# Performance work log

Hardware: AMD Instinct MI355X
Metric: run time of the kernel (lower is better)

## Reference

```python
import jax, jax.numpy as jnp
import numpy as np
from jax import lax
from jax.scipy.special import logsumexp

INSIZE = 256
NBASE = 4
SIZE = 2 * NBASE * (NBASE + 1)  # 40


def setup_inputs() -> dict:
    key = jax.random.key(0)
    kx, kw, kb = jax.random.split(key, 3)
    x = jax.random.normal(kx, (2048, 256, INSIZE), dtype=jnp.float32)
    W = jax.random.normal(kw, (SIZE, INSIZE), dtype=jnp.float32) / np.sqrt(INSIZE)
    b = 0.5 * jax.random.normal(kb, (SIZE,), dtype=jnp.float32)
    return {"x": x, "W": W, "b": b}


def global_norm_flipflop(scores):
    # scores: (T, N, C) with C = 2*nbase*(nbase+1)
    T, N, C = scores.shape
    nbase = int(np.sqrt(C / 2))
    assert 2 * nbase * (nbase + 1) == C

    fwd0 = jnp.zeros((N, 2 * nbase), dtype=scores.dtype)
    logZ0 = logsumexp(fwd0, axis=1, keepdims=True)  # (N, 1) = log(2*nbase)
    fwd0 = fwd0 - logZ0

    def step(carry, sc_t):
        fwd, logZ = carry
        # (N, nbase+1, 2*nbase): transition scores into each destination row
        sc = fwd[:, None, :] + sc_t.reshape(N, nbase + 1, 2 * nbase)
        base1 = logsumexp(sc[:, :nbase], axis=2)  # flip states (N, nbase)
        base2 = jnp.logaddexp(sc[:, nbase, :nbase], sc[:, nbase, nbase:])  # flop (N, nbase)
        new_state = jnp.concatenate([base1, base2], axis=1)  # (N, 2*nbase)
        factors = logsumexp(new_state, axis=1, keepdims=True)
        return (new_state - factors, logZ + factors), None

    (_, logZ), _ = lax.scan(step, (fwd0, logZ0), scores)
    return scores - logZ / T  # broadcast (N,1) over (T,N,C)


def reference(x, W, b):
    y = 5.0 * jnp.tanh(x @ W.T + b)  # (T, N, 40)
    return global_norm_flipflop(y)
```

## Files before the change

kernel.cpp:

```cpp
#include <hip/hip_runtime.h>
#include <hip/hip_bf16.h>

#define T_DIM 2048
#define N_DIM 256
#define K_DIM 256
#define C_DIM 40
#define CHUNK 32
#define NCHUNK 64
#define NSUPER (T_DIM * N_DIM / 64)

#define LOG2E_F 1.44269504088896340736f
#define LN2_F   0.69314718055994530942f
#define NEGBIG  (-1.0e30f)

typedef short bf16x8 __attribute__((ext_vector_type(8)));
typedef float f32x4  __attribute__((ext_vector_type(4)));

__device__ __forceinline__ float fexp2(float x) { return exp2f(x); }
__device__ __forceinline__ float flog2(float x) { return log2f(x); }
__device__ __forceinline__ float frcp(float x) { return __frcp_rn(x); }

__device__ __forceinline__ unsigned int pk2(float a, float b)
{
    __hip_bfloat162 h = __float22bfloat162_rn(make_float2(a, b));
    unsigned int r;
    __builtin_memcpy(&r, &h, sizeof(r));
    return r;
}

__device__ __forceinline__ uint4 pack8u(float4 lo, float4 hi)
{
    uint4 t;
    t.x = pk2(lo.x, lo.y);
    t.y = pk2(lo.z, lo.w);
    t.z = pk2(hi.x, hi.y);
    t.w = pk2(hi.z, hi.w);
    return t;
}

__device__ __forceinline__ bf16x8 as_bf16x8(uint4 u)
{
    bf16x8 r;
    __builtin_memcpy(&r, &u, sizeof(r));
    return r;
}

__device__ __forceinline__ unsigned short bf16r(float v)
{
    return (unsigned short)(pk2(v, 0.0f) & 0xffffu);
}

__device__ __forceinline__ float bl(unsigned int w) { return __uint_as_float(w << 16); }
__device__ __forceinline__ float bh(unsigned int w) { return __uint_as_float(w & 0xffff0000u); }

__device__ __forceinline__ float tanh5(float v)
{
    const float e = fexp2(fabsf(v) * (2.0f * LOG2E_F));
    const float t = 1.0f - 2.0f * frcp(e + 1.0f);
    return 5.0f * copysignf(t, v);
}

__global__ __launch_bounds__(256) void k0_pack(
    const float* __restrict__ W, uint4* __restrict__ wfrag)
{
    const int f    = blockIdx.x * 256 + threadIdx.x;
    const int l    = f & 63;
    const int frag = f >> 6;
    const int nt   = frag % 3;
    const int ks   = frag / 3;
    const int col  = nt * 16 + (l & 15);
    const int kg   = l >> 4;
    float4 lo = make_float4(0, 0, 0, 0), hi = lo;
    if (col < C_DIM) {
        const float* wp = W + (size_t)col * K_DIM + ks * 32 + kg * 8;
        lo = *(const float4*)wp;
        hi = *(const float4*)(wp + 4);
    }
    wfrag[frag * 64 + l] = pack8u(lo, hi);
}

__global__ __launch_bounds__(256, 4) void k1_gemm_tanh(
    const float* __restrict__ x, const uint4* __restrict__ wfrag,
    const float* __restrict__ b, unsigned short* __restrict__ yb)
{
    __shared__ __align__(16) unsigned char xl[64 * 512];

    const int tid  = threadIdx.x;
    const int wave = tid >> 6;
    const int lane = tid & 63;
    const int lr   = lane & 15;
    const int kg   = lane >> 4;
    const int mt   = wave;

    const float bc0 = b[lr];
    const float bc1 = b[16 + lr];
    const float bc2 = (lr < 8) ? b[32 + lr] : 0.0f;

    const int rbase = (mt * 16 + lr) * 512;
    const int swz   = (lr & 7) << 4;

#pragma unroll 1
    for (int st = blockIdx.x; st < NSUPER; st += 1024) {
        const float4* __restrict__ xg4 =
            (const float4*)(x + (size_t)st * 64 * K_DIM);
#pragma unroll
        for (int p = 0; p < 16; ++p) {
            const int f4  = p * 256 + tid;
            const int row = f4 >> 6;
            const int kq  = f4 & 63;
            const float4 v = xg4[f4];
            uint2 w2;
            w2.x = pk2(v.x, v.y);
            w2.y = pk2(v.z, v.w);
            const int off = (row * 512 + kq * 8) ^ ((row & 7) << 4);
            *(uint2*)(xl + off) = w2;
        }
        __syncthreads();

        f32x4 af0 = {bc0, bc0, bc0, bc0};
        f32x4 af1 = {bc1, bc1, bc1, bc1};
        f32x4 af2 = {bc2, bc2, bc2, bc2};

#pragma unroll
        for (int ks = 0; ks < 8; ++ks) {
            const bf16x8 a =
                *(const bf16x8*)(xl + ((rbase + ks * 64 + kg * 16) ^ swz));
            const uint4* wp = wfrag + (ks * 3) * 64 + lane;
            const bf16x8 w0 = as_bf16x8(wp[0]);
            const bf16x8 w1 = as_bf16x8(wp[64]);
            const bf16x8 w2 = as_bf16x8(wp[128]);
            af0 = __builtin_amdgcn_mfma_f32_16x16x32_bf16(a, w0, af0, 0, 0, 0);
            af1 = __builtin_amdgcn_mfma_f32_16x16x32_bf16(a, w1, af1, 0, 0, 0);
            af2 = __builtin_amdgcn_mfma_f32_16x16x32_bf16(a, w2, af2, 0, 0, 0);
        }

        unsigned short* yr =
            yb + ((size_t)st * 64 + mt * 16 + kg * 4) * C_DIM;
#pragma unroll
        for (int r = 0; r < 4; ++r) {
            yr[r * C_DIM + lr]      = bf16r(tanh5(af0[r]));
            yr[r * C_DIM + 16 + lr] = bf16r(tanh5(af1[r]));
            if (lr < 8)
                yr[r * C_DIM + 32 + lr] = bf16r(tanh5(af2[r]));
        }
        __syncthreads();
    }
}

__global__ __launch_bounds__(256) void k2_chunks(
    const unsigned short* __restrict__ yb, float* __restrict__ cmat)
{
    const int tid  = threadIdx.x;
    const int wave = tid >> 6;
    const int lane = tid & 63;
    const int task = lane >> 3;
    const int c    = lane & 7;
    const int g    = blockIdx.x & (NCHUNK - 1);
    const int n    = ((blockIdx.x >> 6) << 5) + (wave << 3) + task;

    float col[8];
#pragma unroll
    for (int j = 0; j < 8; ++j) col[j] = (j == c) ? 0.0f : NEGBIG;

    const unsigned short* __restrict__ yp =
        yb + ((size_t)(g * CHUNK) * N_DIM + (size_t)n) * C_DIM;

#pragma unroll 1
    for (int s = 0; s < CHUNK; ++s) {
        float sc[C_DIM];
        const uint4* p4 = (const uint4*)yp;
#pragma unroll
        for (int q = 0; q < 5; ++q) {
            const uint4 u = p4[q];
            sc[8 * q + 0] = bl(u.x) * LOG2E_F;
            sc[8 * q + 1] = bh(u.x) * LOG2E_F;
            sc[8 * q + 2] = bl(u.y) * LOG2E_F;
            sc[8 * q + 3] = bh(u.y) * LOG2E_F;
            sc[8 * q + 4] = bl(u.z) * LOG2E_F;
            sc[8 * q + 5] = bh(u.z) * LOG2E_F;
            sc[8 * q + 6] = bl(u.w) * LOG2E_F;
            sc[8 * q + 7] = bh(u.w) * LOG2E_F;
        }
        float nc[8];
#pragma unroll
        for (int d = 0; d < 4; ++d) {
            float tv[8];
#pragma unroll
            for (int j = 0; j < 8; ++j) tv[j] = sc[d * 8 + j] + col[j];
            float m = tv[0];
#pragma unroll
            for (int j = 1; j < 8; ++j) m = fmaxf(m, tv[j]);
            float ss = 0.0f;
#pragma unroll
            for (int j = 0; j < 8; ++j) ss += fexp2(tv[j] - m);
            nc[d] = m + flog2(ss);
        }
#pragma unroll
        for (int i = 0; i < 4; ++i) {
            const float a  = sc[32 + i] + col[i];
            const float bb = sc[36 + i] + col[i + 4];
            const float m  = fmaxf(a, bb);
            const float ss = fexp2(a - m) + fexp2(bb - m);
            nc[4 + i] = m + flog2(ss);
        }
#pragma unroll
        for (int j = 0; j < 8; ++j) col[j] = nc[j];
        yp += (size_t)N_DIM * C_DIM;
    }
    float* __restrict__ op = cmat + (((size_t)g * 8 + c) * N_DIM + n) * 8;
#pragma unroll
    for (int j = 0; j < 8; ++j) op[j] = col[j];
}

__global__ __launch_bounds__(256) void k3_combine(
    const float* __restrict__ cmat, float* __restrict__ corr)
{
    const int tid = threadIdx.x;
    const int d   = tid & 7;
    const int n   = blockIdx.x * 32 + (tid >> 3);

    float v[8];
#pragma unroll
    for (int j = 0; j < 8; ++j) v[j] = 0.0f;

#pragma unroll 1
    for (int g = 0; g < NCHUNK; ++g) {
        const float* mg = cmat + ((size_t)g * 8 * N_DIM + n) * 8 + d;
        float mm[8];
#pragma unroll
        for (int j = 0; j < 8; ++j) mm[j] = mg[(size_t)j * N_DIM * 8];
        float tv[8];
#pragma unroll
        for (int j = 0; j < 8; ++j) tv[j] = mm[j] + v[j];
        float m = tv[0];
#pragma unroll
        for (int j = 1; j < 8; ++j) m = fmaxf(m, tv[j]);
        float ss = 0.0f;
#pragma unroll
        for (int j = 0; j < 8; ++j) ss += fexp2(tv[j] - m);
        const float nv = m + flog2(ss);
#pragma unroll
        for (int j = 0; j < 8; ++j) v[j] = __shfl(nv, j, 8);
    }
    float m = v[0];
#pragma unroll
    for (int j = 1; j < 8; ++j) m = fmaxf(m, v[j]);
    float ss = 0.0f;
#pragma unroll
    for (int j = 0; j < 8; ++j) ss += fexp2(v[j] - m);
    const float lz2 = m + flog2(ss);
    if (d == 0) corr[n] = lz2 * LN2_F / (float)T_DIM;
}

__global__ __launch_bounds__(256) void k4_final(
    const unsigned short* __restrict__ yb, const float* __restrict__ corr,
    float* __restrict__ out)
{
    const int i = blockIdx.x * 256 + threadIdx.x;
    const uint4 u = ((const uint4*)yb)[i];
    const float cr = corr[(i / 5) & (N_DIM - 1)];
    float4 o0, o1;
    o0.x = bl(u.x) - cr; o0.y = bh(u.x) - cr;
    o0.z = bl(u.y) - cr; o0.w = bh(u.y) - cr;
    o1.x = bl(u.z) - cr; o1.y = bh(u.z) - cr;
    o1.z = bl(u.w) - cr; o1.w = bh(u.w) - cr;
    float4* o4 = (float4*)out;
    o4[i * 2]     = o0;
    o4[i * 2 + 1] = o1;
}

extern "C" void kernel_launch(void* const* d_in, const int* in_sizes, int n_in,
                              void* d_out, int out_size, void* d_ws, size_t ws_size,
                              hipStream_t stream)
{
    const float* x = (const float*)d_in[0];
    const float* W = (const float*)d_in[1];
    const float* b = (const float*)d_in[2];
    float* out = (float*)d_out;

    unsigned short* ybf = (unsigned short*)d_ws;
    float* cmat = (float*)((char*)d_ws + (48u << 20));
    float* corr = cmat + (size_t)NCHUNK * 8 * N_DIM * 8;
    uint4* wfrag = (uint4*)((char*)d_ws + (56u << 20));

    hipLaunchKernelGGL(k0_pack,      dim3(6),    dim3(256), 0, stream, W, wfrag);
    hipLaunchKernelGGL(k1_gemm_tanh, dim3(1024), dim3(256), 0, stream, x, wfrag, b, ybf);
    hipLaunchKernelGGL(k2_chunks,    dim3(512),  dim3(256), 0, stream, ybf, cmat);
    hipLaunchKernelGGL(k3_combine,   dim3(8),    dim3(256), 0, stream, cmat, corr);
    hipLaunchKernelGGL(k4_final,     dim3(T_DIM * N_DIM * C_DIM / 8 / 256),
                       dim3(256), 0, stream, ybf, corr, out);
}
```

Baseline: 302.6 us.

## Load x directly into MFMA registers and fold W packing into GEMM kernel

The GEMM kernel no longer stages x tiles through LDS with block-wide barriers. Each wave now loads its own 16-row tile straight from global memory into registers, using a K permutation applied consistently to both x and W. W fragment packing moves from a separate launch into each block's shared memory, removing one kernel launch. Blocks grow to 512 threads. This trades LDS traffic and syncs for higher register pressure and less coalesced-per-row global loads.

```diff
diff --git a/kernel.cpp b/kernel.cpp
--- a/kernel.cpp
+++ b/kernel.cpp
@@ -7,7 +7,7 @@
 #define C_DIM 40
 #define CHUNK 32
 #define NCHUNK 64
-#define NSUPER (T_DIM * N_DIM / 64)
+#define NTILES (T_DIM * N_DIM / 16)
 
 #define LOG2E_F 1.44269504088896340736f
 #define LN2_F   0.69314718055994530942f
@@ -60,62 +60,55 @@
     return 5.0f * copysignf(t, v);
 }
 
-__global__ __launch_bounds__(256) void k0_pack(
-    const float* __restrict__ W, uint4* __restrict__ wfrag)
-{
-    const int f    = blockIdx.x * 256 + threadIdx.x;
-    const int l    = f & 63;
-    const int frag = f >> 6;
-    const int nt   = frag % 3;
-    const int ks   = frag / 3;
-    const int col  = nt * 16 + (l & 15);
-    const int kg   = l >> 4;
-    float4 lo = make_float4(0, 0, 0, 0), hi = lo;
-    if (col < C_DIM) {
-        const float* wp = W + (size_t)col * K_DIM + ks * 32 + kg * 8;
-        lo = *(const float4*)wp;
-        hi = *(const float4*)(wp + 4);
-    }
-    wfrag[frag * 64 + l] = pack8u(lo, hi);
-}
-
-__global__ __launch_bounds__(256, 4) void k1_gemm_tanh(
-    const float* __restrict__ x, const uint4* __restrict__ wfrag,
+__global__ __launch_bounds__(512, 4) void k1_gemm_tanh(
+    const float* __restrict__ x, const float* __restrict__ W,
     const float* __restrict__ b, unsigned short* __restrict__ yb)
 {
-    __shared__ __align__(16) unsigned char xl[64 * 512];
-
-    const int tid  = threadIdx.x;
+    __shared__ __align__(16) uint4 wlds[24 * 64];
+
+    const int tid = threadIdx.x;
+
+#pragma unroll
+    for (int p = 0; p < 3; ++p) {
+        const int f    = p * 512 + tid;
+        const int l    = f & 63;
+        const int frag = f >> 6;
+        const int nt   = frag % 3;
+        const int ks   = frag / 3;
+        const int col  = nt * 16 + (l & 15);
+        const int kg   = l >> 4;
+        float4 lo = make_float4(0, 0, 0, 0), hi = lo;
+        if (col < C_DIM) {
+            lo = *(const float4*)(W + (size_t)col * K_DIM + ks * 32 + kg * 4);
+            hi = *(const float4*)(W + (size_t)col * K_DIM + ks * 32 + 16 + kg * 4);
+        }
+        wlds[frag * 64 + l] = pack8u(lo, hi);
+    }
+    __syncthreads();
+
     const int wave = tid >> 6;
     const int lane = tid & 63;
     const int lr   = lane & 15;
     const int kg   = lane >> 4;
-    const int mt   = wave;
 
     const float bc0 = b[lr];
     const float bc1 = b[16 + lr];
     const float bc2 = (lr < 8) ? b[32 + lr] : 0.0f;
 
-    const int rbase = (mt * 16 + lr) * 512;
-    const int swz   = (lr & 7) << 4;
+    const int gw = blockIdx.x * 8 + wave;
 
 #pragma unroll 1
-    for (int st = blockIdx.x; st < NSUPER; st += 1024) {
-        const float4* __restrict__ xg4 =
-            (const float4*)(x + (size_t)st * 64 * K_DIM);
-#pragma unroll
-        for (int p = 0; p < 16; ++p) {
-            const int f4  = p * 256 + tid;
-            const int row = f4 >> 6;
-            const int kq  = f4 & 63;
-            const float4 v = xg4[f4];
-            uint2 w2;
-            w2.x = pk2(v.x, v.y);
-            w2.y = pk2(v.z, v.w);
-            const int off = (row * 512 + kq * 8) ^ ((row & 7) << 4);
-            *(uint2*)(xl + off) = w2;
-        }
-        __syncthreads();
+    for (int tile = gw; tile < NTILES; tile += 4096) {
+        const float4* __restrict__ xp4 =
+            (const float4*)(x + ((size_t)tile * 16 + lr) * K_DIM) + kg;
+
+        float4 lv[16];
+#pragma unroll
+        for (int i = 0; i < 8; ++i) {
+            lv[2 * i]     = xp4[i * 8];
+            lv[2 * i + 1] = xp4[i * 8 + 4];
+        }
+        __builtin_amdgcn_sched_barrier(0);
 
         f32x4 af0 = {bc0, bc0, bc0, bc0};
         f32x4 af1 = {bc1, bc1, bc1, bc1};
@@ -123,19 +116,16 @@
 
 #pragma unroll
         for (int ks = 0; ks < 8; ++ks) {
-            const bf16x8 a =
-                *(const bf16x8*)(xl + ((rbase + ks * 64 + kg * 16) ^ swz));
-            const uint4* wp = wfrag + (ks * 3) * 64 + lane;
-            const bf16x8 w0 = as_bf16x8(wp[0]);
-            const bf16x8 w1 = as_bf16x8(wp[64]);
-            const bf16x8 w2 = as_bf16x8(wp[128]);
+            const bf16x8 a  = as_bf16x8(pack8u(lv[2 * ks], lv[2 * ks + 1]));
+            const bf16x8 w0 = *(const bf16x8*)&wlds[(ks * 3 + 0) * 64 + lane];
+            const bf16x8 w1 = *(const bf16x8*)&wlds[(ks * 3 + 1) * 64 + lane];
+            const bf16x8 w2 = *(const bf16x8*)&wlds[(ks * 3 + 2) * 64 + lane];
             af0 = __builtin_amdgcn_mfma_f32_16x16x32_bf16(a, w0, af0, 0, 0, 0);
             af1 = __builtin_amdgcn_mfma_f32_16x16x32_bf16(a, w1, af1, 0, 0, 0);
             af2 = __builtin_amdgcn_mfma_f32_16x16x32_bf16(a, w2, af2, 0, 0, 0);
         }
 
-        unsigned short* yr =
-            yb + ((size_t)st * 64 + mt * 16 + kg * 4) * C_DIM;
+        unsigned short* yr = yb + ((size_t)tile * 16 + kg * 4) * C_DIM;
 #pragma unroll
         for (int r = 0; r < 4; ++r) {
             yr[r * C_DIM + lr]      = bf16r(tanh5(af0[r]));
@@ -143,7 +133,6 @@
             if (lr < 8)
                 yr[r * C_DIM + 32 + lr] = bf16r(tanh5(af2[r]));
         }
-        __syncthreads();
     }
 }
 
@@ -281,10 +270,8 @@
     unsigned short* ybf = (unsigned short*)d_ws;
     float* cmat = (float*)((char*)d_ws + (48u << 20));
     float* corr = cmat + (size_t)NCHUNK * 8 * N_DIM * 8;
-    uint4* wfrag = (uint4*)((char*)d_ws + (56u << 20));
-
-    hipLaunchKernelGGL(k0_pack,      dim3(6),    dim3(256), 0, stream, W, wfrag);
-    hipLaunchKernelGGL(k1_gemm_tanh, dim3(1024), dim3(256), 0, stream, x, wfrag, b, ybf);
+
+    hipLaunchKernelGGL(k1_gemm_tanh, dim3(512),  dim3(512), 0, stream, x, W, b, ybf);
     hipLaunchKernelGGL(k2_chunks,    dim3(512),  dim3(256), 0, stream, ybf, cmat);
     hipLaunchKernelGGL(k3_combine,   dim3(8),    dim3(256), 0, stream, cmat, corr);
     hipLaunchKernelGGL(k4_final,     dim3(T_DIM * N_DIM * C_DIM / 8 / 256),
```

Result: faster. 262.8 us (-13.1%).
